# Performance work log

Measured on AMD Instinct MI355X. Metric: run time of the kernel, lower is better.

## Reference

```python
import jax, jax.numpy as jnp
import numpy as np

B, S, NQ, D, K = 8, 43, 13, 608, 4  # batch, seq, query nodes, d_model, top-k


def setup_inputs() -> dict:
    key = jax.random.key(0)
    k1, k2, k3 = jax.random.split(key, 3)
    x = jax.random.normal(k1, (B, S, D), dtype=jnp.float32)        # encoder output
    scores = jax.random.normal(k2, (B, S, S), dtype=jnp.float32)   # last-layer attn scores
    W_ff = jax.random.normal(k3, (2 * D, 4), dtype=jnp.float32) * 0.02
    b_ff = jnp.zeros((4,), dtype=jnp.float32)
    return {"x": x, "scores": scores, "W_ff": W_ff, "b_ff": b_ff}


def reference(x, scores, W_ff, b_ff):
    x13 = x[:, :NQ, :]                                   # [B,13,608]
    imp = scores.reshape(-1, S, S)[:, :NQ, :NQ]          # [B,13,13]
    _, idx = jax.lax.top_k(imp, K)                       # [B,13,4] int32, distinct per row
    # gather top-k neighbor features: gathered[b,i,j] = x13[b, idx[b,i,j]]
    gathered = jax.vmap(lambda xb, ib: xb[ib])(x13, idx)            # [B,13,4,608]
    self_feat = jnp.broadcast_to(x13[:, :, None, :], gathered.shape)
    pair = jnp.concatenate([self_feat, gathered], axis=-1)         # [B,13,4,1216]
    vals = pair @ W_ff + b_ff                                       # [B,13,4,4]
    # out initialized to one-hot [1,0,0,0] everywhere, then scatter ff outputs
    base = jnp.zeros((B, NQ, NQ, 4), dtype=jnp.float32).at[..., 0].set(1.0)
    bb = jnp.arange(B)[:, None, None]
    ii = jnp.arange(NQ)[None, :, None]
    out = base.at[bb, ii, idx].set(vals)                            # [B,13,13,4]
    return out
```

## Files before the change

### kernel.cpp

```cpp
#include <hip/hip_runtime.h>

#define NB 8
#define SS 43
#define NQ 13
#define DD 608
#define KK 4
#define NF4 (DD / 4)

__global__ __launch_bounds__(256) void imp_enc_kernel(
    const float* __restrict__ x, const float* __restrict__ scores,
    const float* __restrict__ Wff, const float* __restrict__ bff,
    float* __restrict__ out)
{
    const int bi   = blockIdx.x;
    const int b    = bi / NQ;
    const int i    = bi % NQ;
    const int k    = threadIdx.x >> 6;
    const int lane = threadIdx.x & 63;

    const float4* W4  = (const float4*)Wff;
    const float4* xs4 = (const float4*)(x + ((size_t)b * SS + i) * DD);

    float4 bias = *(const float4*)bff;
    const float* srow = scores + ((size_t)b * SS + i) * SS;
    float myv = (lane < NQ) ? srow[lane] : -INFINITY;

    float accS[4] = {0.f, 0.f, 0.f, 0.f};
    #pragma unroll
    for (int it = 0; it < 3; ++it) {
        const int f = lane + it * 64;
        if (f < NF4) {
            float4 xv = xs4[f];
            const float xe[4] = {xv.x, xv.y, xv.z, xv.w};
            #pragma unroll
            for (int u = 0; u < 4; ++u) {
                float4 wt = W4[f * 4 + u];
                accS[0] += xe[u] * wt.x;
                accS[1] += xe[u] * wt.y;
                accS[2] += xe[u] * wt.z;
                accS[3] += xe[u] * wt.w;
            }
        }
    }

    int rank = 0;
    #pragma unroll
    for (int m = 0; m < NQ; ++m) {
        float vm = __shfl(myv, m, 64);
        if (vm > myv || (vm == myv && m < lane)) ++rank;
    }
    int idx[KK];
    #pragma unroll
    for (int kk = 0; kk < KK; ++kk) {
        unsigned long long msk = __ballot(lane < NQ && rank == kk);
        idx[kk] = (int)__ffsll(msk) - 1;
    }

    const float4* xg4 = (const float4*)(x + ((size_t)b * SS + idx[k]) * DD);
    float accG[4] = {0.f, 0.f, 0.f, 0.f};
    #pragma unroll
    for (int it = 0; it < 3; ++it) {
        const int f = lane + it * 64;
        if (f < NF4) {
            float4 gv = xg4[f];
            const float ge[4] = {gv.x, gv.y, gv.z, gv.w};
            #pragma unroll
            for (int u = 0; u < 4; ++u) {
                float4 wb = W4[DD + f * 4 + u];
                accG[0] += ge[u] * wb.x;
                accG[1] += ge[u] * wb.y;
                accG[2] += ge[u] * wb.z;
                accG[3] += ge[u] * wb.w;
            }
        }
    }

    #pragma unroll
    for (int off = 32; off > 0; off >>= 1) {
        #pragma unroll
        for (int c = 0; c < 4; ++c) {
            accS[c] += __shfl_xor(accS[c], off, 64);
            accG[c] += __shfl_xor(accG[c], off, 64);
        }
    }

    if (lane < NQ * 4) {
        const int j = lane >> 2;
        const int c = lane & 3;
        const float vS = (c & 2) ? ((c & 1) ? accS[3] : accS[2])
                                 : ((c & 1) ? accS[1] : accS[0]);
        const float vG = (c & 2) ? ((c & 1) ? accG[3] : accG[2])
                                 : ((c & 1) ? accG[1] : accG[0]);
        const float bc = (c & 2) ? ((c & 1) ? bias.w : bias.z)
                                 : ((c & 1) ? bias.y : bias.x);
        const bool sel = (j == idx[0]) | (j == idx[1]) | (j == idx[2]) | (j == idx[3]);
        float* orow = out + (size_t)bi * (NQ * 4);
        if (j == idx[k]) {
            orow[lane] = vS + vG + bc;
        } else if (k == 0 && !sel) {
            orow[lane] = (c == 0) ? 1.0f : 0.0f;
        }
    }
}

extern "C" void kernel_launch(void* const* d_in, const int* in_sizes, int n_in,
                              void* d_out, int out_size, void* d_ws, size_t ws_size,
                              hipStream_t stream) {
    const float* x      = (const float*)d_in[0];
    const float* scores = (const float*)d_in[1];
    const float* Wff    = (const float*)d_in[2];
    const float* bff    = (const float*)d_in[3];
    float* out = (float*)d_out;

    imp_enc_kernel<<<NB * NQ, 256, 0, stream>>>(x, scores, Wff, bff, out);
}
```

Baseline: 9.359 us.

## Launch one wavefront per output pair and skip top-k index extraction

The grid changes from one 256-thread block per (b,i) row to one 64-thread wavefront per (b,i,j) output cell, 1352 blocks in total. Each wave computes the self and neighbor dot products for its j in a single fused loop. It decides membership in the top-k with one ballot and popcount instead of a full rank computation plus index extraction. This removes the serial data dependency between top-k and the gather load and exposes more parallelism. In exchange it computes the FF projection for every j, including ones that are not selected (13 instead of 4 per row), and rereads x and W about three times as much.

```diff
diff --git a/kernel.cpp b/kernel.cpp
--- a/kernel.cpp
+++ b/kernel.cpp
@@ -7,73 +7,52 @@
 #define KK 4
 #define NF4 (DD / 4)
 
-__global__ __launch_bounds__(256) void imp_enc_kernel(
+__global__ __launch_bounds__(64) void imp_enc_kernel(
     const float* __restrict__ x, const float* __restrict__ scores,
     const float* __restrict__ Wff, const float* __restrict__ bff,
     float* __restrict__ out)
 {
-    const int bi   = blockIdx.x;
+    const int blk  = blockIdx.x;
+    const int bi   = blk / NQ;
+    const int j    = blk % NQ;
     const int b    = bi / NQ;
     const int i    = bi % NQ;
-    const int k    = threadIdx.x >> 6;
-    const int lane = threadIdx.x & 63;
+    const int lane = threadIdx.x;
 
     const float4* W4  = (const float4*)Wff;
     const float4* xs4 = (const float4*)(x + ((size_t)b * SS + i) * DD);
+    const float4* xj4 = (const float4*)(x + ((size_t)b * SS + j) * DD);
 
     float4 bias = *(const float4*)bff;
     const float* srow = scores + ((size_t)b * SS + i) * SS;
     float myv = (lane < NQ) ? srow[lane] : -INFINITY;
 
     float accS[4] = {0.f, 0.f, 0.f, 0.f};
+    float accG[4] = {0.f, 0.f, 0.f, 0.f};
     #pragma unroll
     for (int it = 0; it < 3; ++it) {
         const int f = lane + it * 64;
         if (f < NF4) {
             float4 xv = xs4[f];
+            float4 gv = xj4[f];
             const float xe[4] = {xv.x, xv.y, xv.z, xv.w};
+            const float ge[4] = {gv.x, gv.y, gv.z, gv.w};
             #pragma unroll
             for (int u = 0; u < 4; ++u) {
                 float4 wt = W4[f * 4 + u];
-                accS[0] += xe[u] * wt.x;
-                accS[1] += xe[u] * wt.y;
-                accS[2] += xe[u] * wt.z;
-                accS[3] += xe[u] * wt.w;
+                float4 wb = W4[DD + f * 4 + u];
+                accS[0] += xe[u] * wt.x;  accG[0] += ge[u] * wb.x;
+                accS[1] += xe[u] * wt.y;  accG[1] += ge[u] * wb.y;
+                accS[2] += xe[u] * wt.z;  accG[2] += ge[u] * wb.z;
+                accS[3] += xe[u] * wt.w;  accG[3] += ge[u] * wb.w;
             }
         }
     }
 
-    int rank = 0;
-    #pragma unroll
-    for (int m = 0; m < NQ; ++m) {
-        float vm = __shfl(myv, m, 64);
-        if (vm > myv || (vm == myv && m < lane)) ++rank;
-    }
-    int idx[KK];
-    #pragma unroll
-    for (int kk = 0; kk < KK; ++kk) {
-        unsigned long long msk = __ballot(lane < NQ && rank == kk);
-        idx[kk] = (int)__ffsll(msk) - 1;
-    }
-
-    const float4* xg4 = (const float4*)(x + ((size_t)b * SS + idx[k]) * DD);
-    float accG[4] = {0.f, 0.f, 0.f, 0.f};
-    #pragma unroll
-    for (int it = 0; it < 3; ++it) {
-        const int f = lane + it * 64;
-        if (f < NF4) {
-            float4 gv = xg4[f];
-            const float ge[4] = {gv.x, gv.y, gv.z, gv.w};
-            #pragma unroll
-            for (int u = 0; u < 4; ++u) {
-                float4 wb = W4[DD + f * 4 + u];
-                accG[0] += ge[u] * wb.x;
-                accG[1] += ge[u] * wb.y;
-                accG[2] += ge[u] * wb.z;
-                accG[3] += ge[u] * wb.w;
-            }
-        }
-    }
+    const float vj = __shfl(myv, j, 64);
+    const unsigned long long better =
+        __ballot(lane < NQ && (myv > vj || (myv == vj && lane < j)));
+    const bool selected = __popcll(better) < KK;
 
     #pragma unroll
     for (int off = 32; off > 0; off >>= 1) {
@@ -84,22 +63,16 @@
         }
     }
 
-    if (lane < NQ * 4) {
-        const int j = lane >> 2;
-        const int c = lane & 3;
+    if (lane < 4) {
+        const int c = lane;
         const float vS = (c & 2) ? ((c & 1) ? accS[3] : accS[2])
                                  : ((c & 1) ? accS[1] : accS[0]);
         const float vG = (c & 2) ? ((c & 1) ? accG[3] : accG[2])
                                  : ((c & 1) ? accG[1] : accG[0]);
         const float bc = (c & 2) ? ((c & 1) ? bias.w : bias.z)
                                  : ((c & 1) ? bias.y : bias.x);
-        const bool sel = (j == idx[0]) | (j == idx[1]) | (j == idx[2]) | (j == idx[3]);
-        float* orow = out + (size_t)bi * (NQ * 4);
-        if (j == idx[k]) {
-            orow[lane] = vS + vG + bc;
-        } else if (k == 0 && !sel) {
-            orow[lane] = (c == 0) ? 1.0f : 0.0f;
-        }
+        const float val = selected ? (vS + vG + bc) : ((c == 0) ? 1.0f : 0.0f);
+        out[(size_t)blk * 4 + c] = val;
     }
 }
 
@@ -112,5 +85,5 @@
     const float* bff    = (const float*)d_in[3];
     float* out = (float*)d_out;
 
-    imp_enc_kernel<<<NB * NQ, 256, 0, stream>>>(x, scores, Wff, bff, out);
+    imp_enc_kernel<<<NB * NQ * NQ, 64, 0, stream>>>(x, scores, Wff, bff, out);
 }
```

Result: slower. 11.68 us (+24.8%).
